# Optimization experiments

Hardware: AMD Instinct MI355X
Metric: run time of the kernel (lower is better)

## Reference

```python
import jax, jax.numpy as jnp
import numpy as np

B, S, E, H, V, C = 256, 20, 512, 512, 32000, 1000


def _lstm_step(x, h, c, W, U, b):
    # Keras LSTM, activation='relu', recurrent_activation='sigmoid', gate order i,f,c,o
    z = x @ W + h @ U + b  # (B, 4H)
    i, f, g, o = jnp.split(z, 4, axis=-1)
    i = jax.nn.sigmoid(i)
    f = jax.nn.sigmoid(f)
    g = jax.nn.relu(g)
    o = jax.nn.sigmoid(o)
    c_new = f * c + i * g
    h_new = o * jax.nn.relu(c_new)
    return h_new, c_new


def setup_inputs() -> dict:
    key = jax.random.key(0)
    ks = jax.random.split(key, 24)
    std = 0.05
    d_in1 = S * E + 2 * E  # flattened encoder output + word embed + speaker embed
    inp = {
        "encoded_output": jax.random.normal(ks[0], (B, S, E), jnp.float32),
        "word_embedding": jax.random.normal(ks[1], (B, E), jnp.float32),
        "h0": jax.random.normal(ks[2], (B, H), jnp.float32) * std,
        "c0": jax.random.normal(ks[3], (B, H), jnp.float32) * std,
        "speaker": jax.random.randint(ks[4], (B,), 0, C),
        "addressee": jax.random.randint(ks[5], (B,), 0, C),
        "persona_emb": jax.random.normal(ks[6], (C, E), jnp.float32) * 0.1,
        "W1": jax.random.normal(ks[7], (d_in1, 4 * H), jnp.float32) * std,
        "U1": jax.random.normal(ks[8], (H, 4 * H), jnp.float32) * std,
        "b1": jnp.zeros((4 * H,), jnp.float32),
        "W2": jax.random.normal(ks[9], (H, 4 * H), jnp.float32) * std,
        "U2": jax.random.normal(ks[10], (H, 4 * H), jnp.float32) * std,
        "b2": jnp.zeros((4 * H,), jnp.float32),
        "W3": jax.random.normal(ks[11], (H, 4 * H), jnp.float32) * std,
        "U3": jax.random.normal(ks[12], (H, 4 * H), jnp.float32) * std,
        "b3": jnp.zeros((4 * H,), jnp.float32),
        "W4": jax.random.normal(ks[13], (H, 4 * H), jnp.float32) * std,
        "U4": jax.random.normal(ks[14], (H, 4 * H), jnp.float32) * std,
        "b4": jnp.zeros((4 * H,), jnp.float32),
        "Wd": jax.random.normal(ks[15], (H, V), jnp.float32) * std,
        "bd": jnp.zeros((V,), jnp.float32),
    }
    return inp


def reference(encoded_output, word_embedding, h0, c0, speaker, addressee,
              persona_emb, W1, U1, b1, W2, U2, b2, W3, U3, b3, W4, U4, b4, Wd, bd):
    b = encoded_output.shape[0]
    # The Python double loop in the original is exactly: (B,S,E) -> (B, S*E)
    enc_flat = encoded_output.reshape(b, -1)
    speaker_embed = persona_emb[speaker]  # (B, E)
    # is_speaker=True branch: concat [flattened encoder, word embed, speaker embed]
    x = jnp.concatenate([enc_flat, word_embedding, speaker_embed], axis=-1)
    # seq length is 1, so each LSTM layer is a single cell step;
    # each layer's initial state is the previous layer's final (h, c)
    h1, c1 = _lstm_step(x, h0, c0, W1, U1, b1)
    h2, c2 = _lstm_step(h1, h1, c1, W2, U2, b2)
    h3, c3 = _lstm_step(h2, h2, c2, W3, U3, b3)
    h4, c4 = _lstm_step(h3, h3, c3, W4, U4, b4)
    probs = jax.nn.softmax(h4 @ Wd + bd, axis=-1)  # (B, V)
    return probs, (h4, c4)
```

## Files before the change

### kernel.cpp

```cpp
#include <hip/hip_runtime.h>
#include <cstdint>
#include <cmath>

typedef _Float16 f16;
typedef _Float16 f16x8 __attribute__((ext_vector_type(8)));
typedef _Float16 f16x4 __attribute__((ext_vector_type(4)));
typedef float f32x4 __attribute__((ext_vector_type(4)));

__device__ inline void gld_lds16(const void* g, void* l) {
  __builtin_amdgcn_global_load_lds(
      (__attribute__((address_space(1))) void*)(uintptr_t)g,
      (__attribute__((address_space(3))) void*)l, 16, 0, 0);
}

__global__ __launch_bounds__(256) void prep_kernel(
    const float* __restrict__ enc, const float* __restrict__ word,
    const float* __restrict__ pers, const int* __restrict__ speaker,
    const float* __restrict__ h0, f16* __restrict__ X,
    const float* __restrict__ W2, const float* __restrict__ U2,
    const float* __restrict__ W3, const float* __restrict__ U3,
    const float* __restrict__ W4, const float* __restrict__ U4,
    f16* __restrict__ wout)
{
  const int job = blockIdx.x;
  if (job < 5888) {
    const int b  = job / 23;
    const int k2 = (job % 23) * 256 + threadIdx.x;
    const int k  = k2 * 2;
    float v0, v1;
    if (k < 10240) {
      const float* p = enc + (long long)b * 10240 + k; v0 = p[0]; v1 = p[1];
    } else if (k < 10752) {
      const float* p = word + b * 512 + (k - 10240);   v0 = p[0]; v1 = p[1];
    } else if (k < 11264) {
      const float* p = pers + (long long)speaker[b] * 512 + (k - 10752); v0 = p[0]; v1 = p[1];
    } else {
      const float* p = h0 + b * 512 + (k - 11264);     v0 = p[0]; v1 = p[1];
    }
    union { f16 h[2]; unsigned int u; } pk;
    pk.h[0] = (f16)v0; pk.h[1] = (f16)v1;
    ((unsigned int*)X)[(long long)b * 5888 + k2] = pk.u;
  } else {
    const int w = job - 5888;
    const int t = (w & 63) * 256 + threadIdx.x;
    const int L = w >> 6;
    const float* W = (L == 0) ? W2 : (L == 1) ? W3 : W4;
    const float* U = (L == 0) ? U2 : (L == 1) ? U3 : U4;
    const int n  = t & 2047;
    const int k0 = (t >> 11) << 6;
    f16* op = wout + (long long)L * (2048 * 512) + (long long)n * 512 + k0;
    for (int kk = 0; kk < 64; kk += 8) {
      f16x8 v;
      #pragma unroll
      for (int j = 0; j < 8; j++) {
        const int k = k0 + kk + j;
        v[j] = (f16)(W[(long long)k * 2048 + n] + U[(long long)k * 2048 + n]);
      }
      *(f16x8*)(op + kk) = v;
    }
  }
}

__global__ __launch_bounds__(256, 2) void gemm_pipe2(
    const f16* __restrict__ A, int lda,
    const float* __restrict__ B0, const float* __restrict__ B1, int ksw, int ldb,
    void* __restrict__ Cv, int ldc, long long c_split_stride, int niter,
    int store_f16, int NT, int NS)
{
  __shared__ __align__(16) f16 Ah[2][256 * 32];
  __shared__ __align__(16) f16 Bh[2][128 * 40];

  const int f   = blockIdx.x;
  const int xcd = f & 7;
  const int j   = f >> 3;
  int nt, s;
  if (NS > 1) {
    const int g = j / NT;
    nt = j - g * NT;
    s  = g * 8 + xcd;
    if (s >= NS) return;
  } else {
    const int chunk = (NT + 7) >> 3;
    if (j >= chunk) return;
    nt = xcd * chunk + j;
    if (nt >= NT) return;
    s = 0;
  }

  const int phase = (f * 7) & (niter - 1);
  auto rot = [&](int kt) {
    int x = kt + phase;
    if (x >= niter) x -= niter;
    return x;
  };

  const int tid  = threadIdx.x;
  const int lane = tid & 63;
  const int wave = tid >> 6;
  const int n0 = nt * 128;
  const int kbeg = s * (niter * 32);

  const int a_row16 = lane >> 2;
  const int a_ksub  = ((lane & 3) ^ ((lane >> 3) & 3)) * 8;

  const int nl0  = (tid & 63) * 2;
  const int koct = tid >> 6;

  float2 bv[8];

  auto issueB = [&](int kt) {
    const int kb = kbeg + rot(kt) * 32 + koct * 8;
    #pragma unroll
    for (int i = 0; i < 8; i++) {
      const int krow = kb + i;
      const float* bp = (krow >= ksw) ? (B1 + (long long)(krow - ksw) * ldb)
                                      : (B0 + (long long)krow * ldb);
      bv[i] = *(const float2*)(bp + n0 + nl0);
    }
  };
  auto issueA = [&](int kt) {
    const int akb = kbeg + rot(kt) * 32;
    #pragma unroll
    for (int half = 0; half < 4; half++) {
      const int rb = wave * 64 + half * 16;
      const f16* gp = A + (long long)(rb + a_row16) * lda + akb + a_ksub;
      gld_lds16((const void*)gp, (void*)&Ah[kt & 1][rb * 32]);
    }
  };
  auto writeB = [&](int kt) {
    f16x8 p0, p1;
    #pragma unroll
    for (int i = 0; i < 8; i++) { p0[i] = (f16)bv[i].x; p1[i] = (f16)bv[i].y; }
    *(f16x8*)&Bh[kt & 1][(nl0    ) * 40 + koct * 8] = p0;
    *(f16x8*)&Bh[kt & 1][(nl0 + 1) * 40 + koct * 8] = p1;
  };

  const int wm = (wave & 1) * 128;
  const int wn = (wave >> 1) * 64;
  f32x4 acc[8][4] = {};

  issueB(0); issueA(0); writeB(0);
  __syncthreads();

  for (int kt = 0; kt < niter; kt++) {
    const int buf = kt & 1;
    const bool more = (kt + 1 < niter);
    if (more) { issueB(kt + 1); issueA(kt + 1); }

    f16x8 bf[4];
    #pragma unroll
    for (int ni = 0; ni < 4; ni++) {
      const int n = wn + ni * 16 + (lane & 15);
      bf[ni] = *(const f16x8*)&Bh[buf][n * 40 + (lane >> 4) * 8];
    }
    #pragma unroll
    for (int mi = 0; mi < 8; mi++) {
      const int m = wm + mi * 16 + (lane & 15);
      const f16x8 af = *(const f16x8*)&Ah[buf][m * 32 + (((lane >> 4) ^ ((m >> 1) & 3)) * 8)];
      #pragma unroll
      for (int ni = 0; ni < 4; ni++)
        acc[mi][ni] = __builtin_amdgcn_mfma_f32_16x16x32_f16(af, bf[ni], acc[mi][ni], 0, 0, 0);
    }

    if (more) writeB(kt + 1);
    __syncthreads();
  }

  if (store_f16) {
    f16* Cs = (f16*)Cv + (long long)s * c_split_stride;
    #pragma unroll
    for (int mi = 0; mi < 8; mi++) {
      const int r0 = wm + mi * 16 + (lane >> 4) * 4;
      #pragma unroll
      for (int ni = 0; ni < 4; ni++) {
        const int cc = n0 + wn + ni * 16 + (lane & 15);
        #pragma unroll
        for (int r = 0; r < 4; r++)
          Cs[(long long)(r0 + r) * ldc + cc] = (f16)acc[mi][ni][r];
      }
    }
  } else {
    float* Cs = (float*)Cv + (long long)s * c_split_stride;
    #pragma unroll
    for (int mi = 0; mi < 8; mi++) {
      const int r0 = wm + mi * 16 + (lane >> 4) * 4;
      #pragma unroll
      for (int ni = 0; ni < 4; ni++) {
        const int cc = n0 + wn + ni * 16 + (lane & 15);
        #pragma unroll
        for (int r = 0; r < 4; r++)
          Cs[(long long)(r0 + r) * ldc + cc] = acc[mi][ni][r];
      }
    }
  }
}

__global__ __launch_bounds__(64) void lstm_small_layer(
    const f16* __restrict__ h_in,
    const f16* __restrict__ WsT,
    const float* __restrict__ bias,
    const float* __restrict__ c_prev, float* __restrict__ c_out,
    f16* __restrict__ h16_out, float* __restrict__ h32_out)
{
  const int lane = threadIdx.x;
  const int wid  = blockIdx.x;
  const int jt = wid & 31, mt = wid >> 5;
  const int m0 = mt * 16, j0 = jt * 16;
  const int lj = lane & 15, quad = lane >> 4;

  const f16* Ab = h_in + (long long)(m0 + lj) * 512 + quad * 8;
  const f16* Bb = WsT + (long long)(j0 + lj) * 512 + quad * 8;
  const long long GS = 512LL * 512;

  f32x4 g0 = {}, g1 = {}, g2 = {}, g3 = {};

  f16x8 ca = *(const f16x8*)(Ab);
  f16x8 cb0 = *(const f16x8*)(Bb);
  f16x8 cb1 = *(const f16x8*)(Bb + GS);
  f16x8 cb2 = *(const f16x8*)(Bb + 2 * GS);
  f16x8 cb3 = *(const f16x8*)(Bb + 3 * GS);

  #pragma unroll
  for (int kt = 0; kt < 16; kt++) {
    f16x8 na = ca, nb0 = cb0, nb1 = cb1, nb2 = cb2, nb3 = cb3;
    if (kt < 15) {
      const int k = (kt + 1) * 32;
      na  = *(const f16x8*)(Ab + k);
      nb0 = *(const f16x8*)(Bb + k);
      nb1 = *(const f16x8*)(Bb + GS + k);
      nb2 = *(const f16x8*)(Bb + 2 * GS + k);
      nb3 = *(const f16x8*)(Bb + 3 * GS + k);
    }
    g0 = __builtin_amdgcn_mfma_f32_16x16x32_f16(ca, cb0, g0, 0, 0, 0);
    g1 = __builtin_amdgcn_mfma_f32_16x16x32_f16(ca, cb1, g1, 0, 0, 0);
    g2 = __builtin_amdgcn_mfma_f32_16x16x32_f16(ca, cb2, g2, 0, 0, 0);
    g3 = __builtin_amdgcn_mfma_f32_16x16x32_f16(ca, cb3, g3, 0, 0, 0);
    ca = na; cb0 = nb0; cb1 = nb1; cb2 = nb2; cb3 = nb3;
  }

  const float bi = bias[j0 + lj],        bfv = bias[512 + j0 + lj];
  const float bg = bias[1024 + j0 + lj], bo  = bias[1536 + j0 + lj];
  #pragma unroll
  for (int r = 0; r < 4; r++) {
    const int m = m0 + quad * 4 + r;
    const int idx = m * 512 + j0 + lj;
    const float gi = 1.f / (1.f + expf(-(g0[r] + bi)));
    const float gf = 1.f / (1.f + expf(-(g1[r] + bfv)));
    const float gg = fmaxf(g2[r] + bg, 0.f);
    const float go = 1.f / (1.f + expf(-(g3[r] + bo)));
    const float cn = gf * c_prev[idx] + gi * gg;
    const float hn = go * fmaxf(cn, 0.f);
    c_out[idx] = cn;
    h16_out[idx] = (f16)hn;
    if (h32_out) h32_out[idx] = hn;
  }
}

__global__ __launch_bounds__(256) void gate_kernel(
    const unsigned int* __restrict__ zbase, int nsplit,
    const float* __restrict__ bias,
    const float* __restrict__ c_prev, float* __restrict__ c_out,
    f16* __restrict__ h16_out)
{
  const int idx2 = blockIdx.x * 256 + threadIdx.x;
  const int b  = idx2 >> 8;
  const int j2 = idx2 & 255;
  const int j  = j2 * 2;
  float z[4][2];
  #pragma unroll
  for (int g = 0; g < 4; g++) { z[g][0] = bias[g * 512 + j]; z[g][1] = bias[g * 512 + j + 1]; }
  #pragma unroll 2
  for (int s = 0; s < nsplit; s++) {
    const unsigned int* zp = zbase + (long long)s * 262144 + b * 1024;
    #pragma unroll
    for (int g = 0; g < 4; g++) {
      union { unsigned int u; f16 h[2]; } v;
      v.u = zp[g * 256 + j2];
      z[g][0] += (float)v.h[0];
      z[g][1] += (float)v.h[1];
    }
  }
  #pragma unroll
  for (int e = 0; e < 2; e++) {
    const float gi = 1.f / (1.f + expf(-z[0][e]));
    const float gf = 1.f / (1.f + expf(-z[1][e]));
    const float gg = fmaxf(z[2][e], 0.f);
    const float go = 1.f / (1.f + expf(-z[3][e]));
    const int idx = b * 512 + j + e;
    const float cn = gf * c_prev[idx] + gi * gg;
    const float hn = go * fmaxf(cn, 0.f);
    c_out[idx] = cn;
    h16_out[idx] = (f16)hn;
  }
}

__global__ __launch_bounds__(1024) void softmax_kernel(
    const f16* __restrict__ zdec, float* __restrict__ out,
    const float* __restrict__ bd)
{
  const int row = blockIdx.x;
  const int t = threadIdx.x;
  const f16x4* p0 = (const f16x4*)(zdec + (long long)row * 32000);
  float4* rp = (float4*)(out + (long long)row * 32000);
  const float4* bp = (const float4*)bd;
  float4 l[8];
  float m = -1e30f;
  #pragma unroll
  for (int i = 0; i < 8; i++) {
    const int v = t + i * 1024;
    if (v < 8000) {
      const f16x4 a = p0[v];
      const float4 bb = bp[v];
      float4 x;
      x.x = (float)a[0] + bb.x;
      x.y = (float)a[1] + bb.y;
      x.z = (float)a[2] + bb.z;
      x.w = (float)a[3] + bb.w;
      l[i] = x;
      m = fmaxf(m, fmaxf(fmaxf(x.x, x.y), fmaxf(x.z, x.w)));
    } else {
      l[i] = make_float4(-1e30f, -1e30f, -1e30f, -1e30f);
    }
  }
  #pragma unroll
  for (int off = 32; off > 0; off >>= 1) m = fmaxf(m, __shfl_xor(m, off, 64));
  __shared__ float redm[16];
  __shared__ float reds[16];
  const int w = t >> 6;
  if ((t & 63) == 0) redm[w] = m;
  __syncthreads();
  float bm = redm[0];
  #pragma unroll
  for (int i = 1; i < 16; i++) bm = fmaxf(bm, redm[i]);
  float s = 0.f;
  #pragma unroll
  for (int i = 0; i < 8; i++) {
    const float ex = expf(l[i].x - bm), ey = expf(l[i].y - bm);
    const float ez = expf(l[i].z - bm), ew = expf(l[i].w - bm);
    l[i] = make_float4(ex, ey, ez, ew);
    s += (ex + ey) + (ez + ew);
  }
  #pragma unroll
  for (int off = 32; off > 0; off >>= 1) s += __shfl_xor(s, off, 64);
  if ((t & 63) == 0) reds[w] = s;
  __syncthreads();
  float ts = 0.f;
  #pragma unroll
  for (int i = 0; i < 16; i++) ts += reds[i];
  const float inv = 1.0f / ts;
  #pragma unroll
  for (int i = 0; i < 8; i++) {
    const int v = t + i * 1024;
    if (v < 8000) {
      float4 x = l[i];
      x.x *= inv; x.y *= inv; x.z *= inv; x.w *= inv;
      rp[v] = x;
    }
  }
}

extern "C" void kernel_launch(void* const* d_in, const int* in_sizes, int n_in,
                              void* d_out, int out_size, void* d_ws, size_t ws_size,
                              hipStream_t stream) {
  const float* enc     = (const float*)d_in[0];
  const float* word    = (const float*)d_in[1];
  const float* h0      = (const float*)d_in[2];
  const float* c0      = (const float*)d_in[3];
  const int*   speaker = (const int*)d_in[4];
  const float* pers = (const float*)d_in[6];
  const float* W1 = (const float*)d_in[7];
  const float* U1 = (const float*)d_in[8];
  const float* b1 = (const float*)d_in[9];
  const float* W2 = (const float*)d_in[10];
  const float* U2 = (const float*)d_in[11];
  const float* b2 = (const float*)d_in[12];
  const float* W3 = (const float*)d_in[13];
  const float* U3 = (const float*)d_in[14];
  const float* b3 = (const float*)d_in[15];
  const float* W4 = (const float*)d_in[16];
  const float* U4 = (const float*)d_in[17];
  const float* b4 = (const float*)d_in[18];
  const float* Wd = (const float*)d_in[19];
  const float* bd = (const float*)d_in[20];

  float* out = (float*)d_out;
  float* h4_out = out + 8192000;
  float* c4_out = out + 8192000 + 131072;

  f16*   hA   = (f16*)d_ws;
  f16*   hB   = (f16*)((char*)d_ws + 262144);
  f16*   hC   = (f16*)((char*)d_ws + 524288);
  float* cbuf = (float*)((char*)d_ws + 786432);
  f16*   WsT  = (f16*)((char*)d_ws + 2097152);
  f16*   X1h  = (f16*)((char*)d_ws + 8388608);
  f16*   zp16 = (f16*)((char*)d_ws + 16777216);
  f16*   zdec = (f16*)((char*)d_ws + 50331648);

  const int BIG = 1 << 29;
  const long long LW = 2048LL * 512;

  prep_kernel<<<dim3(6080), 256, 0, stream>>>(
      enc, word, pers, speaker, h0, X1h, W2, U2, W3, U3, W4, U4, WsT);

  gemm_pipe2<<<dim3(384), 256, 0, stream>>>(
      X1h, 11776, W1, U1, 11264, 2048, zp16, 2048, 524288LL, 16, 1, 16, 23);
  gate_kernel<<<dim3(256), 256, 0, stream>>>((const unsigned int*)zp16, 23, b1, c0, cbuf, hA);

  lstm_small_layer<<<dim3(512), 64, 0, stream>>>(hA, WsT,          b2, cbuf, cbuf, hB, nullptr);
  lstm_small_layer<<<dim3(512), 64, 0, stream>>>(hB, WsT + LW,     b3, cbuf, cbuf, hA, nullptr);
  lstm_small_layer<<<dim3(512), 64, 0, stream>>>(hA, WsT + 2 * LW, b4, cbuf, c4_out, hC, h4_out);

  gemm_pipe2<<<dim3(256), 256, 0, stream>>>(
      hC, 512, Wd, Wd, BIG, 32000, zdec, 32000, 0LL, 16, 1, 250, 1);

  softmax_kernel<<<dim3(256), 1024, 0, stream>>>(zdec, out, bd);
}
```

Before: 349.6 us.

## Fuse LSTM stages and decoder+softmax into persistent kernels with grid barriers

Merges the layer-1 split-K GEMM, gate reduction and three small LSTM layers into one persistent kernel separated by atomic-counter grid barriers. The decoder GEMM and softmax are merged the same way. The goal is to remove five kernel launches and the gaps between them. The costs are that the k-phase rotation is dropped, the softmax now runs on 256-thread blocks that re-read the logits three times and recompute exp, and correctness relies on all blocks being co-resident.

```diff
diff --git a/kernel.cpp b/kernel.cpp
--- a/kernel.cpp
+++ b/kernel.cpp
@@ -11,6 +11,18 @@
   __builtin_amdgcn_global_load_lds(
       (__attribute__((address_space(1))) void*)(uintptr_t)g,
       (__attribute__((address_space(3))) void*)l, 16, 0, 0);
+}
+
+__device__ inline void gbar(int* cnt, int nblk) {
+  __syncthreads();
+  __threadfence();
+  if (threadIdx.x == 0) {
+    __hip_atomic_fetch_add(cnt, 1, __ATOMIC_ACQ_REL, __HIP_MEMORY_SCOPE_AGENT);
+    while (__hip_atomic_load(cnt, __ATOMIC_ACQUIRE, __HIP_MEMORY_SCOPE_AGENT) < nblk)
+      __builtin_amdgcn_s_sleep(8);
+  }
+  __syncthreads();
+  __threadfence();
 }
 
 __global__ __launch_bounds__(256) void prep_kernel(
@@ -20,9 +32,10 @@
     const float* __restrict__ W2, const float* __restrict__ U2,
     const float* __restrict__ W3, const float* __restrict__ U3,
     const float* __restrict__ W4, const float* __restrict__ U4,
-    f16* __restrict__ wout)
+    f16* __restrict__ wout, int* __restrict__ cnts)
 {
   const int job = blockIdx.x;
+  if (job == 0 && threadIdx.x < 8) cnts[threadIdx.x] = 0;
   if (job < 5888) {
     const int b  = job / 23;
     const int k2 = (job % 23) * 256 + threadIdx.x;
@@ -61,149 +74,13 @@
   }
 }
 
-__global__ __launch_bounds__(256, 2) void gemm_pipe2(
-    const f16* __restrict__ A, int lda,
-    const float* __restrict__ B0, const float* __restrict__ B1, int ksw, int ldb,
-    void* __restrict__ Cv, int ldc, long long c_split_stride, int niter,
-    int store_f16, int NT, int NS)
-{
-  __shared__ __align__(16) f16 Ah[2][256 * 32];
-  __shared__ __align__(16) f16 Bh[2][128 * 40];
-
-  const int f   = blockIdx.x;
-  const int xcd = f & 7;
-  const int j   = f >> 3;
-  int nt, s;
-  if (NS > 1) {
-    const int g = j / NT;
-    nt = j - g * NT;
-    s  = g * 8 + xcd;
-    if (s >= NS) return;
-  } else {
-    const int chunk = (NT + 7) >> 3;
-    if (j >= chunk) return;
-    nt = xcd * chunk + j;
-    if (nt >= NT) return;
-    s = 0;
-  }
-
-  const int phase = (f * 7) & (niter - 1);
-  auto rot = [&](int kt) {
-    int x = kt + phase;
-    if (x >= niter) x -= niter;
-    return x;
-  };
-
-  const int tid  = threadIdx.x;
-  const int lane = tid & 63;
-  const int wave = tid >> 6;
-  const int n0 = nt * 128;
-  const int kbeg = s * (niter * 32);
-
-  const int a_row16 = lane >> 2;
-  const int a_ksub  = ((lane & 3) ^ ((lane >> 3) & 3)) * 8;
-
-  const int nl0  = (tid & 63) * 2;
-  const int koct = tid >> 6;
-
-  float2 bv[8];
-
-  auto issueB = [&](int kt) {
-    const int kb = kbeg + rot(kt) * 32 + koct * 8;
-    #pragma unroll
-    for (int i = 0; i < 8; i++) {
-      const int krow = kb + i;
-      const float* bp = (krow >= ksw) ? (B1 + (long long)(krow - ksw) * ldb)
-                                      : (B0 + (long long)krow * ldb);
-      bv[i] = *(const float2*)(bp + n0 + nl0);
-    }
-  };
-  auto issueA = [&](int kt) {
-    const int akb = kbeg + rot(kt) * 32;
-    #pragma unroll
-    for (int half = 0; half < 4; half++) {
-      const int rb = wave * 64 + half * 16;
-      const f16* gp = A + (long long)(rb + a_row16) * lda + akb + a_ksub;
-      gld_lds16((const void*)gp, (void*)&Ah[kt & 1][rb * 32]);
-    }
-  };
-  auto writeB = [&](int kt) {
-    f16x8 p0, p1;
-    #pragma unroll
-    for (int i = 0; i < 8; i++) { p0[i] = (f16)bv[i].x; p1[i] = (f16)bv[i].y; }
-    *(f16x8*)&Bh[kt & 1][(nl0    ) * 40 + koct * 8] = p0;
-    *(f16x8*)&Bh[kt & 1][(nl0 + 1) * 40 + koct * 8] = p1;
-  };
-
-  const int wm = (wave & 1) * 128;
-  const int wn = (wave >> 1) * 64;
-  f32x4 acc[8][4] = {};
-
-  issueB(0); issueA(0); writeB(0);
-  __syncthreads();
-
-  for (int kt = 0; kt < niter; kt++) {
-    const int buf = kt & 1;
-    const bool more = (kt + 1 < niter);
-    if (more) { issueB(kt + 1); issueA(kt + 1); }
-
-    f16x8 bf[4];
-    #pragma unroll
-    for (int ni = 0; ni < 4; ni++) {
-      const int n = wn + ni * 16 + (lane & 15);
-      bf[ni] = *(const f16x8*)&Bh[buf][n * 40 + (lane >> 4) * 8];
-    }
-    #pragma unroll
-    for (int mi = 0; mi < 8; mi++) {
-      const int m = wm + mi * 16 + (lane & 15);
-      const f16x8 af = *(const f16x8*)&Ah[buf][m * 32 + (((lane >> 4) ^ ((m >> 1) & 3)) * 8)];
-      #pragma unroll
-      for (int ni = 0; ni < 4; ni++)
-        acc[mi][ni] = __builtin_amdgcn_mfma_f32_16x16x32_f16(af, bf[ni], acc[mi][ni], 0, 0, 0);
-    }
-
-    if (more) writeB(kt + 1);
-    __syncthreads();
-  }
-
-  if (store_f16) {
-    f16* Cs = (f16*)Cv + (long long)s * c_split_stride;
-    #pragma unroll
-    for (int mi = 0; mi < 8; mi++) {
-      const int r0 = wm + mi * 16 + (lane >> 4) * 4;
-      #pragma unroll
-      for (int ni = 0; ni < 4; ni++) {
-        const int cc = n0 + wn + ni * 16 + (lane & 15);
-        #pragma unroll
-        for (int r = 0; r < 4; r++)
-          Cs[(long long)(r0 + r) * ldc + cc] = (f16)acc[mi][ni][r];
-      }
-    }
-  } else {
-    float* Cs = (float*)Cv + (long long)s * c_split_stride;
-    #pragma unroll
-    for (int mi = 0; mi < 8; mi++) {
-      const int r0 = wm + mi * 16 + (lane >> 4) * 4;
-      #pragma unroll
-      for (int ni = 0; ni < 4; ni++) {
-        const int cc = n0 + wn + ni * 16 + (lane & 15);
-        #pragma unroll
-        for (int r = 0; r < 4; r++)
-          Cs[(long long)(r0 + r) * ldc + cc] = acc[mi][ni][r];
-      }
-    }
-  }
-}
-
-__global__ __launch_bounds__(64) void lstm_small_layer(
-    const f16* __restrict__ h_in,
-    const f16* __restrict__ WsT,
+__device__ void lstm_tile(
+    int wid, int lane,
+    const f16* __restrict__ h_in, const f16* __restrict__ WsT,
     const float* __restrict__ bias,
     const float* __restrict__ c_prev, float* __restrict__ c_out,
     f16* __restrict__ h16_out, float* __restrict__ h32_out)
 {
-  const int lane = threadIdx.x;
-  const int wid  = blockIdx.x;
   const int jt = wid & 31, mt = wid >> 5;
   const int m0 = mt * 16, j0 = jt * 16;
   const int lj = lane & 15, quad = lane >> 4;
@@ -256,105 +133,297 @@
   }
 }
 
-__global__ __launch_bounds__(256) void gate_kernel(
-    const unsigned int* __restrict__ zbase, int nsplit,
-    const float* __restrict__ bias,
-    const float* __restrict__ c_prev, float* __restrict__ c_out,
-    f16* __restrict__ h16_out)
+__global__ __launch_bounds__(256, 2) void mid_kernel(
+    const f16* __restrict__ X1h, const float* __restrict__ W1,
+    const float* __restrict__ U1, f16* __restrict__ zp16,
+    const float* __restrict__ b1, const float* __restrict__ c0,
+    float* __restrict__ cbuf, f16* __restrict__ hA, f16* __restrict__ hB,
+    f16* __restrict__ hC, const f16* __restrict__ WsT,
+    const float* __restrict__ b2, const float* __restrict__ b3,
+    const float* __restrict__ b4, float* __restrict__ c4_out,
+    float* __restrict__ h4_out, int* __restrict__ cnts)
 {
-  const int idx2 = blockIdx.x * 256 + threadIdx.x;
-  const int b  = idx2 >> 8;
-  const int j2 = idx2 & 255;
-  const int j  = j2 * 2;
-  float z[4][2];
-  #pragma unroll
-  for (int g = 0; g < 4; g++) { z[g][0] = bias[g * 512 + j]; z[g][1] = bias[g * 512 + j + 1]; }
-  #pragma unroll 2
-  for (int s = 0; s < nsplit; s++) {
-    const unsigned int* zp = zbase + (long long)s * 262144 + b * 1024;
+  __shared__ __align__(16) f16 Ah[2][256 * 32];
+  __shared__ __align__(16) f16 Bh[2][128 * 40];
+
+  const int tid  = threadIdx.x;
+  const int lane = tid & 63;
+  const int wave = tid >> 6;
+
+  {
+    const int f   = blockIdx.x;
+    const int xcd = f & 7;
+    const int j   = f >> 3;
+    const int g   = j >> 4;
+    const int nt  = j & 15;
+    const int s   = g * 8 + xcd;
+    if (s < 23) {
+      const int n0 = nt * 128;
+      const int kbeg = s * 512;
+      const int a_row16 = lane >> 2;
+      const int a_ksub  = ((lane & 3) ^ ((lane >> 3) & 3)) * 8;
+      const int nl0  = lane * 2;
+      const int koct = wave;
+
+      float2 bv[8];
+      auto issueB = [&](int kt) {
+        const int kb = kbeg + kt * 32 + koct * 8;
+        #pragma unroll
+        for (int i = 0; i < 8; i++) {
+          const int krow = kb + i;
+          const float* bp = (krow >= 11264) ? (U1 + (long long)(krow - 11264) * 2048)
+                                            : (W1 + (long long)krow * 2048);
+          bv[i] = *(const float2*)(bp + n0 + nl0);
+        }
+      };
+      auto issueA = [&](int kt) {
+        const int akb = kbeg + kt * 32;
+        #pragma unroll
+        for (int half = 0; half < 4; half++) {
+          const int rb = wave * 64 + half * 16;
+          const f16* gp = X1h + (long long)(rb + a_row16) * 11776 + akb + a_ksub;
+          gld_lds16((const void*)gp, (void*)&Ah[kt & 1][rb * 32]);
+        }
+      };
+      auto writeB = [&](int kt) {
+        f16x8 p0, p1;
+        #pragma unroll
+        for (int i = 0; i < 8; i++) { p0[i] = (f16)bv[i].x; p1[i] = (f16)bv[i].y; }
+        *(f16x8*)&Bh[kt & 1][(nl0    ) * 40 + koct * 8] = p0;
+        *(f16x8*)&Bh[kt & 1][(nl0 + 1) * 40 + koct * 8] = p1;
+      };
+
+      const int wm = (wave & 1) * 128;
+      const int wn = (wave >> 1) * 64;
+      f32x4 acc[8][4] = {};
+
+      issueB(0); issueA(0); writeB(0);
+      __syncthreads();
+      for (int kt = 0; kt < 16; kt++) {
+        const int buf = kt & 1;
+        const bool more = (kt + 1 < 16);
+        if (more) { issueB(kt + 1); issueA(kt + 1); }
+        f16x8 bf[4];
+        #pragma unroll
+        for (int ni = 0; ni < 4; ni++) {
+          const int n = wn + ni * 16 + (lane & 15);
+          bf[ni] = *(const f16x8*)&Bh[buf][n * 40 + (lane >> 4) * 8];
+        }
+        #pragma unroll
+        for (int mi = 0; mi < 8; mi++) {
+          const int m = wm + mi * 16 + (lane & 15);
+          const f16x8 af = *(const f16x8*)&Ah[buf][m * 32 + (((lane >> 4) ^ ((m >> 1) & 3)) * 8)];
+          #pragma unroll
+          for (int ni = 0; ni < 4; ni++)
+            acc[mi][ni] = __builtin_amdgcn_mfma_f32_16x16x32_f16(af, bf[ni], acc[mi][ni], 0, 0, 0);
+        }
+        if (more) writeB(kt + 1);
+        __syncthreads();
+      }
+      f16* Cs = zp16 + (long long)s * 524288;
+      #pragma unroll
+      for (int mi = 0; mi < 8; mi++) {
+        const int r0 = wm + mi * 16 + (lane >> 4) * 4;
+        #pragma unroll
+        for (int ni = 0; ni < 4; ni++) {
+          const int cc = n0 + wn + ni * 16 + (lane & 15);
+          #pragma unroll
+          for (int r = 0; r < 4; r++)
+            Cs[(long long)(r0 + r) * 2048 + cc] = (f16)acc[mi][ni][r];
+        }
+      }
+    }
+  }
+  gbar(&cnts[0], 384);
+
+  {
+    const int idx2 = blockIdx.x * 256 + tid;
+    if (idx2 < 65536) {
+      const unsigned int* zb = (const unsigned int*)zp16;
+      const int b  = idx2 >> 8;
+      const int j2 = idx2 & 255;
+      const int jj = j2 * 2;
+      float z[4][2];
+      #pragma unroll
+      for (int g = 0; g < 4; g++) { z[g][0] = b1[g * 512 + jj]; z[g][1] = b1[g * 512 + jj + 1]; }
+      #pragma unroll 2
+      for (int s = 0; s < 23; s++) {
+        const unsigned int* zp = zb + (long long)s * 262144 + b * 1024;
+        #pragma unroll
+        for (int g = 0; g < 4; g++) {
+          union { unsigned int u; f16 h[2]; } v;
+          v.u = zp[g * 256 + j2];
+          z[g][0] += (float)v.h[0];
+          z[g][1] += (float)v.h[1];
+        }
+      }
+      #pragma unroll
+      for (int e = 0; e < 2; e++) {
+        const float gi = 1.f / (1.f + expf(-z[0][e]));
+        const float gf = 1.f / (1.f + expf(-z[1][e]));
+        const float gg = fmaxf(z[2][e], 0.f);
+        const float go = 1.f / (1.f + expf(-z[3][e]));
+        const int idx = b * 512 + jj + e;
+        const float cn = gf * c0[idx] + gi * gg;
+        const float hn = go * fmaxf(cn, 0.f);
+        cbuf[idx] = cn;
+        hA[idx] = (f16)hn;
+      }
+    }
+  }
+  gbar(&cnts[1], 384);
+
+  const long long LW = 2048LL * 512;
+  const int wid = blockIdx.x * 4 + wave;
+  if (wid < 512) lstm_tile(wid, lane, hA, WsT,          b2, cbuf, cbuf, hB, nullptr);
+  gbar(&cnts[2], 384);
+  if (wid < 512) lstm_tile(wid, lane, hB, WsT + LW,     b3, cbuf, cbuf, hA, nullptr);
+  gbar(&cnts[3], 384);
+  if (wid < 512) lstm_tile(wid, lane, hA, WsT + 2 * LW, b4, cbuf, c4_out, hC, h4_out);
+}
+
+__global__ __launch_bounds__(256, 2) void dec_kernel(
+    const f16* __restrict__ hC, const float* __restrict__ Wd,
+    f16* __restrict__ zdec, const float* __restrict__ bd,
+    float* __restrict__ out, int* __restrict__ cnts)
+{
+  __shared__ __align__(16) f16 Ah[2][256 * 32];
+  __shared__ __align__(16) f16 Bh[2][128 * 40];
+  __shared__ float redA[4];
+  __shared__ float redB[4];
+
+  const int tid  = threadIdx.x;
+  const int lane = tid & 63;
+  const int wave = tid >> 6;
+
+  {
+    const int f   = blockIdx.x;
+    const int xcd = f & 7;
+    const int j   = f >> 3;
+    const int nt  = xcd * 32 + j;
+    if (nt < 250) {
+      const int n0 = nt * 128;
+      const int a_row16 = lane >> 2;
+      const int a_ksub  = ((lane & 3) ^ ((lane >> 3) & 3)) * 8;
+      const int nl0  = lane * 2;
+      const int koct = wave;
+
+      float2 bv[8];
+      auto issueB = [&](int kt) {
+        const int kb = kt * 32 + koct * 8;
+        #pragma unroll
+        for (int i = 0; i < 8; i++) {
+          const float* bp = Wd + (long long)(kb + i) * 32000;
+          bv[i] = *(const float2*)(bp + n0 + nl0);
+        }
+      };
+      auto issueA = [&](int kt) {
+        const int akb = kt * 32;
+        #pragma unroll
+        for (int half = 0; half < 4; half++) {
+          const int rb = wave * 64 + half * 16;
+          const f16* gp = hC + (long long)(rb + a_row16) * 512 + akb + a_ksub;
+          gld_lds16((const void*)gp, (void*)&Ah[kt & 1][rb * 32]);
+        }
+      };
+      auto writeB = [&](int kt) {
+        f16x8 p0, p1;
+        #pragma unroll
+        for (int i = 0; i < 8; i++) { p0[i] = (f16)bv[i].x; p1[i] = (f16)bv[i].y; }
+        *(f16x8*)&Bh[kt & 1][(nl0    ) * 40 + koct * 8] = p0;
+        *(f16x8*)&Bh[kt & 1][(nl0 + 1) * 40 + koct * 8] = p1;
+      };
+
+      const int wm = (wave & 1) * 128;
+      const int wn = (wave >> 1) * 64;
+      f32x4 acc[8][4] = {};
+
+      issueB(0); issueA(0); writeB(0);
+      __syncthreads();
+      for (int kt = 0; kt < 16; kt++) {
+        const int buf = kt & 1;
+        const bool more = (kt + 1 < 16);
+        if (more) { issueB(kt + 1); issueA(kt + 1); }
+        f16x8 bf[4];
+        #pragma unroll
+        for (int ni = 0; ni < 4; ni++) {
+          const int n = wn + ni * 16 + (lane & 15);
+          bf[ni] = *(const f16x8*)&Bh[buf][n * 40 + (lane >> 4) * 8];
+        }
+        #pragma unroll
+        for (int mi = 0; mi < 8; mi++) {
+          const int m = wm + mi * 16 + (lane & 15);
+          const f16x8 af = *(const f16x8*)&Ah[buf][m * 32 + (((lane >> 4) ^ ((m >> 1) & 3)) * 8)];
+          #pragma unroll
+          for (int ni = 0; ni < 4; ni++)
+            acc[mi][ni] = __builtin_amdgcn_mfma_f32_16x16x32_f16(af, bf[ni], acc[mi][ni], 0, 0, 0);
+        }
+        if (more) writeB(kt + 1);
+        __syncthreads();
+      }
+      #pragma unroll
+      for (int mi = 0; mi < 8; mi++) {
+        const int r0 = wm + mi * 16 + (lane >> 4) * 4;
+        #pragma unroll
+        for (int ni = 0; ni < 4; ni++) {
+          const int cc = n0 + wn + ni * 16 + (lane & 15);
+          #pragma unroll
+          for (int r = 0; r < 4; r++)
+            zdec[(long long)(r0 + r) * 32000 + cc] = (f16)acc[mi][ni][r];
+        }
+      }
+    }
+  }
+  gbar(&cnts[4], 256);
+
+  {
+    const int row = blockIdx.x;
+    const f16x4* zp = (const f16x4*)(zdec + (long long)row * 32000);
+    const float4* bp = (const float4*)bd;
+    float4* rp = (float4*)(out + (long long)row * 32000);
+
+    float m = -1e30f;
+    for (int i = 0; i < 32; i++) {
+      const int v = tid + i * 256;
+      if (v < 8000) {
+        const f16x4 a = zp[v]; const float4 bb = bp[v];
+        const float x0 = (float)a[0] + bb.x, x1 = (float)a[1] + bb.y;
+        const float x2 = (float)a[2] + bb.z, x3 = (float)a[3] + bb.w;
+        m = fmaxf(m, fmaxf(fmaxf(x0, x1), fmaxf(x2, x3)));
+      }
+    }
     #pragma unroll
-    for (int g = 0; g < 4; g++) {
-      union { unsigned int u; f16 h[2]; } v;
-      v.u = zp[g * 256 + j2];
-      z[g][0] += (float)v.h[0];
-      z[g][1] += (float)v.h[1];
-    }
-  }
-  #pragma unroll
-  for (int e = 0; e < 2; e++) {
-    const float gi = 1.f / (1.f + expf(-z[0][e]));
-    const float gf = 1.f / (1.f + expf(-z[1][e]));
-    const float gg = fmaxf(z[2][e], 0.f);
-    const float go = 1.f / (1.f + expf(-z[3][e]));
-    const int idx = b * 512 + j + e;
-    const float cn = gf * c_prev[idx] + gi * gg;
-    const float hn = go * fmaxf(cn, 0.f);
-    c_out[idx] = cn;
-    h16_out[idx] = (f16)hn;
-  }
-}
-
-__global__ __launch_bounds__(1024) void softmax_kernel(
-    const f16* __restrict__ zdec, float* __restrict__ out,
-    const float* __restrict__ bd)
-{
-  const int row = blockIdx.x;
-  const int t = threadIdx.x;
-  const f16x4* p0 = (const f16x4*)(zdec + (long long)row * 32000);
-  float4* rp = (float4*)(out + (long long)row * 32000);
-  const float4* bp = (const float4*)bd;
-  float4 l[8];
-  float m = -1e30f;
-  #pragma unroll
-  for (int i = 0; i < 8; i++) {
-    const int v = t + i * 1024;
-    if (v < 8000) {
-      const f16x4 a = p0[v];
-      const float4 bb = bp[v];
-      float4 x;
-      x.x = (float)a[0] + bb.x;
-      x.y = (float)a[1] + bb.y;
-      x.z = (float)a[2] + bb.z;
-      x.w = (float)a[3] + bb.w;
-      l[i] = x;
-      m = fmaxf(m, fmaxf(fmaxf(x.x, x.y), fmaxf(x.z, x.w)));
-    } else {
-      l[i] = make_float4(-1e30f, -1e30f, -1e30f, -1e30f);
-    }
-  }
-  #pragma unroll
-  for (int off = 32; off > 0; off >>= 1) m = fmaxf(m, __shfl_xor(m, off, 64));
-  __shared__ float redm[16];
-  __shared__ float reds[16];
-  const int w = t >> 6;
-  if ((t & 63) == 0) redm[w] = m;
-  __syncthreads();
-  float bm = redm[0];
-  #pragma unroll
-  for (int i = 1; i < 16; i++) bm = fmaxf(bm, redm[i]);
-  float s = 0.f;
-  #pragma unroll
-  for (int i = 0; i < 8; i++) {
-    const float ex = expf(l[i].x - bm), ey = expf(l[i].y - bm);
-    const float ez = expf(l[i].z - bm), ew = expf(l[i].w - bm);
-    l[i] = make_float4(ex, ey, ez, ew);
-    s += (ex + ey) + (ez + ew);
-  }
-  #pragma unroll
-  for (int off = 32; off > 0; off >>= 1) s += __shfl_xor(s, off, 64);
-  if ((t & 63) == 0) reds[w] = s;
-  __syncthreads();
-  float ts = 0.f;
-  #pragma unroll
-  for (int i = 0; i < 16; i++) ts += reds[i];
-  const float inv = 1.0f / ts;
-  #pragma unroll
-  for (int i = 0; i < 8; i++) {
-    const int v = t + i * 1024;
-    if (v < 8000) {
-      float4 x = l[i];
-      x.x *= inv; x.y *= inv; x.z *= inv; x.w *= inv;
-      rp[v] = x;
+    for (int off = 32; off > 0; off >>= 1) m = fmaxf(m, __shfl_xor(m, off, 64));
+    if (lane == 0) redA[wave] = m;
+    __syncthreads();
+    const float bm = fmaxf(fmaxf(redA[0], redA[1]), fmaxf(redA[2], redA[3]));
+
+    float s = 0.f;
+    for (int i = 0; i < 32; i++) {
+      const int v = tid + i * 256;
+      if (v < 8000) {
+        const f16x4 a = zp[v]; const float4 bb = bp[v];
+        s += expf((float)a[0] + bb.x - bm) + expf((float)a[1] + bb.y - bm)
+           + expf((float)a[2] + bb.z - bm) + expf((float)a[3] + bb.w - bm);
+      }
+    }
+    #pragma unroll
+    for (int off = 32; off > 0; off >>= 1) s += __shfl_xor(s, off, 64);
+    if (lane == 0) redB[wave] = s;
+    __syncthreads();
+    const float inv = 1.0f / (redB[0] + redB[1] + redB[2] + redB[3]);
+
+    for (int i = 0; i < 32; i++) {
+      const int v = tid + i * 256;
+      if (v < 8000) {
+        const f16x4 a = zp[v]; const float4 bb = bp[v];
+        float4 x;
+        x.x = expf((float)a[0] + bb.x - bm) * inv;
+        x.y = expf((float)a[1] + bb.y - bm) * inv;
+        x.z = expf((float)a[2] + bb.z - bm) * inv;
+        x.w = expf((float)a[3] + bb.w - bm) * inv;
+        rp[v] = x;
+      }
     }
   }
 }
@@ -391,27 +460,18 @@
   f16*   hB   = (f16*)((char*)d_ws + 262144);
   f16*   hC   = (f16*)((char*)d_ws + 524288);
   float* cbuf = (float*)((char*)d_ws + 786432);
+  int*   cnts = (int*)((char*)d_ws + 1310720);
   f16*   WsT  = (f16*)((char*)d_ws + 2097152);
   f16*   X1h  = (f16*)((char*)d_ws + 8388608);
   f16*   zp16 = (f16*)((char*)d_ws + 16777216);
   f16*   zdec = (f16*)((char*)d_ws + 50331648);
 
-  const int BIG = 1 << 29;
-  const long long LW = 2048LL * 512;
-
   prep_kernel<<<dim3(6080), 256, 0, stream>>>(
-      enc, word, pers, speaker, h0, X1h, W2, U2, W3, U3, W4, U4, WsT);
-
-  gemm_pipe2<<<dim3(384), 256, 0, stream>>>(
-      X1h, 11776, W1, U1, 11264, 2048, zp16, 2048, 524288LL, 16, 1, 16, 23);
-  gate_kernel<<<dim3(256), 256, 0, stream>>>((const unsigned int*)zp16, 23, b1, c0, cbuf, hA);
-
-  lstm_small_layer<<<dim3(512), 64, 0, stream>>>(hA, WsT,          b2, cbuf, cbuf, hB, nullptr);
-  lstm_small_layer<<<dim3(512), 64, 0, stream>>>(hB, WsT + LW,     b3, cbuf, cbuf, hA, nullptr);
-  lstm_small_layer<<<dim3(512), 64, 0, stream>>>(hA, WsT + 2 * LW, b4, cbuf, c4_out, hC, h4_out);
-
-  gemm_pipe2<<<dim3(256), 256, 0, stream>>>(
-      hC, 512, Wd, Wd, BIG, 32000, zdec, 32000, 0LL, 16, 1, 250, 1);
-
-  softmax_kernel<<<dim3(256), 1024, 0, stream>>>(zdec, out, bd);
-}
+      enc, word, pers, speaker, h0, X1h, W2, U2, W3, U3, W4, U4, WsT, cnts);
+
+  mid_kernel<<<dim3(384), 256, 0, stream>>>(
+      X1h, W1, U1, zp16, b1, c0, cbuf, hA, hB, hC, WsT, b2, b3, b4,
+      c4_out, h4_out, cnts);
+
+  dec_kernel<<<dim3(256), 256, 0, stream>>>(hC, Wd, zdec, bd, out, cnts);
+}
```

Result: slower. 1.008 ms (+188.3%).
